# Performance work log

Measured on AMD Instinct MI355X. Metric: run time of the kernel, lower is better.

The kernel has to match this reference:

```python
import jax, jax.numpy as jnp
import numpy as np

N_NODES = 50000
N_EDGES = 800000
NUM_GRAPHS = 256
F_IN = 64        # num_features (per-head out dim == in dim in this module)
HEADS = 4        # n_heads1
OUT_DIM = 128    # output_dim
HC = HEADS * F_IN
NEG_SLOPE = 0.2  # GATConv leaky_relu slope
EPS = 1e-5       # GraphNorm eps


def setup_inputs() -> dict:
    key = jax.random.key(0)
    ks = jax.random.split(key, 12)
    s = lambda k, shape, fan: (jax.random.normal(k, shape, jnp.float32) / np.sqrt(fan).astype(np.float32))
    return {
        "x": jax.random.normal(ks[0], (N_NODES, F_IN), jnp.float32),
        "edge_index": jax.random.randint(ks[1], (2, N_EDGES), 0, N_NODES),
        "batch": jnp.sort(jax.random.randint(ks[2], (N_NODES,), 0, NUM_GRAPHS)),
        # GATConv params
        "lin_w": s(ks[3], (HC, F_IN), F_IN),
        "att_src": s(ks[4], (HEADS, F_IN), F_IN),
        "att_dst": s(ks[5], (HEADS, F_IN), F_IN),
        "gat_bias": jnp.zeros((HC,), jnp.float32),
        # GraphNorm params
        "gn_weight": jnp.ones((HC,), jnp.float32),
        "gn_bias": jnp.zeros((HC,), jnp.float32),
        "gn_mean_scale": jnp.ones((HC,), jnp.float32),
        # fc_g1 / out heads
        "fc1_w": s(ks[6], (OUT_DIM, HC), HC), "fc1_b": jnp.zeros((OUT_DIM,), jnp.float32),
        "out_w": s(ks[7], (1, OUT_DIM), OUT_DIM), "out_b": jnp.zeros((1,), jnp.float32),
        # GlobalAttention gate_nn: Linear(HC,16) -> ReLU -> Linear(16,1) -> Sigmoid
        "att1_w": s(ks[8], (16, HC), HC), "att1_b": jnp.zeros((16,), jnp.float32),
        "att2_w": s(ks[9], (1, 16), 16), "att2_b": jnp.zeros((1,), jnp.float32),
    }


def _gat_conv(x, edge_index, lin_w, att_src, att_dst, gat_bias):
    """PyG GATConv with add_self_loops=True, concat heads. Returns (out [N,HC], alpha [E+N,H])."""
    N = x.shape[0]
    xh = (x @ lin_w.T).reshape(N, HEADS, F_IN)                 # [N,H,C]
    a_src = (xh * att_src[None]).sum(-1)                        # [N,H]
    a_dst = (xh * att_dst[None]).sum(-1)                        # [N,H]
    loops = jnp.arange(N)
    src = jnp.concatenate([edge_index[0], loops])               # [E+N]
    dst = jnp.concatenate([edge_index[1], loops])
    alpha = jax.nn.leaky_relu(a_src[src] + a_dst[dst], NEG_SLOPE)  # [E+N,H]
    # segment softmax over incoming edges of each dst node (self-loops guarantee non-empty)
    amax = jax.ops.segment_max(alpha, dst, num_segments=N)
    alpha = jnp.exp(alpha - amax[dst])
    denom = jax.ops.segment_sum(alpha, dst, num_segments=N)
    alpha = alpha / (denom[dst] + 1e-16)
    msg = xh[src] * alpha[:, :, None]                           # [E+N,H,C]
    out = jax.ops.segment_sum(msg, dst, num_segments=N).reshape(N, HC) + gat_bias
    return out, alpha


def _graph_norm(x, batch, weight, bias, mean_scale):
    ones = jnp.ones((x.shape[0],), x.dtype)
    cnt = jnp.maximum(jax.ops.segment_sum(ones, batch, num_segments=NUM_GRAPHS), 1.0)[:, None]
    mean = jax.ops.segment_sum(x, batch, num_segments=NUM_GRAPHS) / cnt
    sub = x - mean[batch] * mean_scale
    var = jax.ops.segment_sum(sub * sub, batch, num_segments=NUM_GRAPHS) / cnt
    return weight * sub / jnp.sqrt(var + EPS)[batch] + bias


def _global_attention(x, batch, att1_w, att1_b, att2_w, att2_b):
    gate = jax.nn.sigmoid(jax.nn.relu(x @ att1_w.T + att1_b) @ att2_w.T + att2_b)  # [N,1]
    gmax = jax.ops.segment_max(gate, batch, num_segments=NUM_GRAPHS)
    gate = jnp.exp(gate - gmax[batch])
    gden = jax.ops.segment_sum(gate, batch, num_segments=NUM_GRAPHS)
    gate = gate / (gden[batch] + 1e-16)
    return jax.ops.segment_sum(gate * x, batch, num_segments=NUM_GRAPHS)  # [G,HC]


def reference(x, edge_index, batch, lin_w, att_src, att_dst, gat_bias,
              gn_weight, gn_bias, gn_mean_scale, fc1_w, fc1_b, out_w, out_b,
              att1_w, att1_b, att2_w, att2_b):
    x2, alpha = _gat_conv(x, edge_index, lin_w, att_src, att_dst, gat_bias)
    h = _graph_norm(x2, batch, gn_weight, gn_bias, gn_mean_scale)
    h = jax.nn.relu(h)                                # node_dropout = identity (eval)
    pooled = _global_attention(h, batch, att1_w, att1_b, att2_w, att2_b)
    h = jax.nn.relu(pooled @ fc1_w.T + fc1_b)          # dropout = identity (eval)
    out = jax.nn.sigmoid(h @ out_w.T + out_b)          # [G,1]
    return out, alpha
```

## Files before the change

### kernel.cpp

```cpp
#include <hip/hip_runtime.h>
#include <hip/hip_fp16.h>
#include <math.h>

#define NN 50000
#define NE 800000
#define NG 256
#define NEG_SLOPE 0.2f
#define GEPS 1e-5f
#define CHUNK 64
#define NB 196
#define CAP 6144
#define EPB 3125
#define SPLIT 8
#define NLINB 782
#define ABLK 3321

typedef _Float16 f16x8 __attribute__((ext_vector_type(8)));
typedef _Float16 f16x4 __attribute__((ext_vector_type(4)));
typedef float f32x4 __attribute__((ext_vector_type(4)));
typedef float f32x2 __attribute__((ext_vector_type(2)));

__device__ __forceinline__ float lrelu(float v){ return v > 0.f ? v : NEG_SLOPE * v; }

__global__ __launch_bounds__(256) void k_misc(const float* __restrict__ lin_w,
                                              _Float16* __restrict__ wh,
                                              const float* __restrict__ att1_w,
                                              _Float16* __restrict__ a1w,
                                              const int* __restrict__ batch,
                                              int* __restrict__ goff,
                                              int* __restrict__ gcnt,
                                              int* __restrict__ bucket_cnt) {
  int b = blockIdx.x, tid = threadIdx.x;
  if (b == 0) {
    if (tid < NB) bucket_cnt[tid] = 0;
    int g = tid;
    int lo = 0, hi = NN;
    while (lo < hi) { int mid = (lo + hi) >> 1; if (batch[mid] < g) lo = mid + 1; else hi = mid; }
    int start = lo;
    lo = 0; hi = NN;
    while (lo < hi) { int mid = (lo + hi) >> 1; if (batch[mid] < g + 1) lo = mid + 1; else hi = mid; }
    goff[g] = start;
    gcnt[g] = lo - start;
  } else if (b <= 16) {
    int i0 = (b - 1) * 1024 + tid * 4;
    float4 f = *(const float4*)&lin_w[i0];
    f16x4 h4;
    h4[0] = (_Float16)f.x; h4[1] = (_Float16)f.y; h4[2] = (_Float16)f.z; h4[3] = (_Float16)f.w;
    *(f16x4*)&wh[i0] = h4;
  } else {
    int i0 = (b - 17) * 1024 + tid * 4;
    float4 f = *(const float4*)&att1_w[i0];
    f16x4 h4;
    h4[0] = (_Float16)f.x; h4[1] = (_Float16)f.y; h4[2] = (_Float16)f.z; h4[3] = (_Float16)f.w;
    *(f16x4*)&a1w[i0] = h4;
  }
}

__device__ __forceinline__ void lin_body(char* smem,
                                         const float* __restrict__ x,
                                         const _Float16* __restrict__ wh,
                                         const float* __restrict__ att_src,
                                         const float* __restrict__ att_dst,
                                         unsigned char* __restrict__ xh8,
                                         float* __restrict__ a_src_n,
                                         float* __restrict__ a_dst_n) {
  unsigned char* s_f8 = (unsigned char*)smem;
  int w = threadIdx.x >> 6, lane = threadIdx.x & 63;
  int nb = blockIdx.x * 64 + w * 16;
  if (nb >= NN) return;
  int am = lane & 15, quad = lane >> 4;
  int wb = w * 4096;

  const float* xr = x + (size_t)(nb + am) * 64 + quad * 8;
  float4 f0 = *(const float4*)(xr);
  float4 f1 = *(const float4*)(xr + 4);
  float4 f2 = *(const float4*)(xr + 32);
  float4 f3 = *(const float4*)(xr + 36);
  f16x8 a0, a1;
  a0[0] = (_Float16)f0.x; a0[1] = (_Float16)f0.y; a0[2] = (_Float16)f0.z; a0[3] = (_Float16)f0.w;
  a0[4] = (_Float16)f1.x; a0[5] = (_Float16)f1.y; a0[6] = (_Float16)f1.z; a0[7] = (_Float16)f1.w;
  a1[0] = (_Float16)f2.x; a1[1] = (_Float16)f2.y; a1[2] = (_Float16)f2.z; a1[3] = (_Float16)f2.w;
  a1[4] = (_Float16)f3.x; a1[5] = (_Float16)f3.y; a1[6] = (_Float16)f3.z; a1[7] = (_Float16)f3.w;

  f32x4 acc[16];
#pragma unroll
  for (int ct = 0; ct < 16; ct++) acc[ct] = (f32x4){0.f, 0.f, 0.f, 0.f};

#pragma unroll
  for (int ct = 0; ct < 16; ct++) {
    const _Float16* wbp = wh + (size_t)(ct * 16 + am) * 64 + quad * 8;
    f16x8 b0 = *(const f16x8*)(wbp);
    f16x8 b1 = *(const f16x8*)(wbp + 32);
    acc[ct] = __builtin_amdgcn_mfma_f32_16x16x32_f16(a0, b0, acc[ct], 0, 0, 0);
    acc[ct] = __builtin_amdgcn_mfma_f32_16x16x32_f16(a1, b1, acc[ct], 0, 0, 0);
  }

  float ps[4][4], pd[4][4];
#pragma unroll
  for (int r = 0; r < 4; r++)
#pragma unroll
    for (int h = 0; h < 4; h++) { ps[r][h] = 0.f; pd[r][h] = 0.f; }
#pragma unroll
  for (int ct = 0; ct < 16; ct++) {
    int c = ct * 16 + am;
    float av = att_src[c];
    float dv = att_dst[c];
    int h = ct >> 2;
#pragma unroll
    for (int r = 0; r < 4; r++) {
      float v = acc[ct][r];
      ps[r][h] += v * av;
      pd[r][h] += v * dv;
    }
  }
#pragma unroll
  for (int r = 0; r < 4; r++)
#pragma unroll
    for (int h = 0; h < 4; h++) {
      float s = ps[r][h], d = pd[r][h];
#pragma unroll
      for (int o = 1; o < 16; o <<= 1) {
        s += __shfl_xor(s, o, 64);
        d += __shfl_xor(d, o, 64);
      }
      if (am == 0) {
        int node = nb + quad * 4 + r;
        a_src_n[node * 4 + h] = s;
        a_dst_n[node * 4 + h] = d;
      }
    }

#pragma unroll
  for (int r = 0; r < 4; r++) {
    uint4 u;
    int t;
    t = __builtin_amdgcn_cvt_pk_fp8_f32(acc[0][r],  acc[1][r],  0, 0);
    t = __builtin_amdgcn_cvt_pk_fp8_f32(acc[2][r],  acc[3][r],  t, 1);
    u.x = (unsigned)t;
    t = __builtin_amdgcn_cvt_pk_fp8_f32(acc[4][r],  acc[5][r],  0, 0);
    t = __builtin_amdgcn_cvt_pk_fp8_f32(acc[6][r],  acc[7][r],  t, 1);
    u.y = (unsigned)t;
    t = __builtin_amdgcn_cvt_pk_fp8_f32(acc[8][r],  acc[9][r],  0, 0);
    t = __builtin_amdgcn_cvt_pk_fp8_f32(acc[10][r], acc[11][r], t, 1);
    u.z = (unsigned)t;
    t = __builtin_amdgcn_cvt_pk_fp8_f32(acc[12][r], acc[13][r], 0, 0);
    t = __builtin_amdgcn_cvt_pk_fp8_f32(acc[14][r], acc[15][r], t, 1);
    u.w = (unsigned)t;
    *(uint4*)&s_f8[wb + (quad * 4 + r) * 256 + am * 16] = u;
  }
#pragma unroll
  for (int p = 0; p < 4; p++) {
    uint4 u = *(const uint4*)&s_f8[wb + p * 1024 + lane * 16];
    *(uint4*)&xh8[(size_t)nb * 256 + p * 1024 + lane * 16] = u;
  }
}

__device__ __forceinline__ void binA_body(char* smem, int b,
                                          const int* __restrict__ ei,
                                          int* __restrict__ bucket_cnt,
                                          int2* __restrict__ ebuf) {
  int2* sorted = (int2*)smem;
  int*  hist   = (int*)(smem + 25024);
  int*  lbase  = (int*)(smem + 25824);
  int*  cur    = (int*)(smem + 26624);
  int*  runb   = (int*)(smem + 27424);
  int*  wsum   = (int*)(smem + 28224);
  int tid = threadIdx.x, lane = tid & 63, wid = tid >> 6;
  int e0 = b * EPB, e1 = min(e0 + EPB, NE);
  int n = e1 - e0;
  for (int i = tid; i < NB; i += 256) hist[i] = 0;
  __syncthreads();
  for (int e = e0 + tid; e < e1; e += 256) atomicAdd(&hist[ei[NE + e] >> 8], 1);
  __syncthreads();
  {
    int v = (tid < NB) ? hist[tid] : 0;
    int s = v;
#pragma unroll
    for (int o = 1; o < 64; o <<= 1) { int t = __shfl_up(s, o, 64); if (lane >= o) s += t; }
    if (lane == 63) wsum[wid] = s;
    __syncthreads();
    int wbase = 0;
    for (int k = 0; k < wid; k++) wbase += wsum[k];
    if (tid < NB) {
      int ex = wbase + s - v;
      lbase[tid] = ex;
      cur[tid] = ex;
      runb[tid] = atomicAdd(&bucket_cnt[tid], v);
    }
  }
  __syncthreads();
  for (int e = e0 + tid; e < e1; e += 256) {
    int d = ei[NE + e], s = ei[e];
    int lp = atomicAdd(&cur[d >> 8], 1);
    sorted[lp] = make_int2(d, s);
  }
  __syncthreads();
  for (int i = tid; i < n; i += 256) {
    int2 e = sorted[i];
    int bk = e.x >> 8;
    int slot = runb[bk] + (i - lbase[bk]);
    if (slot < CAP) ebuf[(size_t)bk * CAP + slot] = e;
  }
}

__global__ __launch_bounds__(256) void k_linbin(const float* __restrict__ x,
                                                const _Float16* __restrict__ wh,
                                                const float* __restrict__ att_src,
                                                const float* __restrict__ att_dst,
                                                unsigned char* __restrict__ xh8,
                                                float* __restrict__ a_src_n,
                                                float* __restrict__ a_dst_n,
                                                const int* __restrict__ ei,
                                                int* __restrict__ bucket_cnt,
                                                int2* __restrict__ ebuf) {
  __shared__ __align__(16) char smem[28240];
  if (blockIdx.x < NLINB)
    lin_body(smem, x, wh, att_src, att_dst, xh8, a_src_n, a_dst_n);
  else
    binA_body(smem, blockIdx.x - NLINB, ei, bucket_cnt, ebuf);
}

__global__ __launch_bounds__(256) void k_binB(const int2* __restrict__ ebuf,
                                              const int* __restrict__ bucket_cnt,
                                              int* __restrict__ deg,
                                              int* __restrict__ offs,
                                              int* __restrict__ src_list) {
  __shared__ int hist[256];
  __shared__ int cur[256];
  __shared__ int wsum[4];
  __shared__ int bbase[NB];
  int b = blockIdx.x, tid = threadIdx.x, lane = tid & 63, wid = tid >> 6;
  {
    int v = (tid < NB) ? min(bucket_cnt[tid], CAP) : 0;
    int s = v;
#pragma unroll
    for (int o = 1; o < 64; o <<= 1) { int t = __shfl_up(s, o, 64); if (lane >= o) s += t; }
    if (lane == 63) wsum[wid] = s;
    __syncthreads();
    int wbase = 0;
    for (int k = 0; k < wid; k++) wbase += wsum[k];
    if (tid < NB) bbase[tid] = wbase + s - v;
  }
  __syncthreads();
  int cnt = min(bucket_cnt[b], CAP);
  int base = bbase[b];
  const int2* seg = ebuf + (size_t)b * CAP;
  hist[tid] = 0;
  __syncthreads();
  for (int i = tid; i < cnt; i += 256) atomicAdd(&hist[seg[i].x & 255], 1);
  __syncthreads();
  int v = hist[tid];
  int s = v;
#pragma unroll
  for (int o = 1; o < 64; o <<= 1) { int t = __shfl_up(s, o, 64); if (lane >= o) s += t; }
  if (lane == 63) wsum[wid] = s;
  __syncthreads();
  int wbase = 0;
  for (int k = 0; k < wid; k++) wbase += wsum[k];
  int excl = wbase + s - v;
  int node = b * 256 + tid;
  if (node < NN) {
    deg[node] = v;
    offs[node] = base + excl;
  }
  cur[tid] = excl;
  __syncthreads();
  for (int i = tid; i < cnt; i += 256) {
    int2 e = seg[i];
    int pos = base + atomicAdd(&cur[e.x & 255], 1);
    src_list[pos] = e.y;
  }
}

__global__ __launch_bounds__(64) void k_gat(const unsigned char* __restrict__ xh8,
                                            const float* __restrict__ a_src_n,
                                            const float* __restrict__ a_dst_n,
                                            const int* __restrict__ offs,
                                            const int* __restrict__ deg_arr,
                                            const int* __restrict__ src_list,
                                            const float* __restrict__ gat_bias,
                                            __half* __restrict__ x2h,
                                            float* __restrict__ den_inv) {
  __shared__ __align__(16) float s_al[CHUNK * 4];
  __shared__ int s_src[CHUNK];
  __shared__ __half s_tr[256];
  int n = blockIdx.x, lane = threadIdx.x;
  int off = offs[n], dg = deg_arr[n], cnt = dg + 1;
  float4 ad = *(const float4*)&a_dst_n[n * 4];
  int h = lane & 3;
  unsigned loff = 4u * (unsigned)lane;
  float acc0 = 0.f, acc1 = 0.f, acc2 = 0.f, acc3 = 0.f;

  if (cnt <= 64) {
    float e0 = 0.f, e1 = 0.f, e2 = 0.f, e3 = 0.f;
    if (lane < cnt) {
      int src = (lane < dg) ? src_list[off + lane] : n;
      float4 as = *(const float4*)&a_src_n[src * 4];
      e0 = __expf(lrelu(as.x + ad.x));
      e1 = __expf(lrelu(as.y + ad.y));
      e2 = __expf(lrelu(as.z + ad.z));
      e3 = __expf(lrelu(as.w + ad.w));
      s_src[lane] = src;
    }
    float s0 = e0, s1 = e1, s2 = e2, s3 = e3;
#pragma unroll
    for (int o = 32; o >= 1; o >>= 1) {
      s0 += __shfl_xor(s0, o, 64);
      s1 += __shfl_xor(s1, o, 64);
      s2 += __shfl_xor(s2, o, 64);
      s3 += __shfl_xor(s3, o, 64);
    }
    float i0 = 1.f / (s0 + 1e-16f), i1 = 1.f / (s1 + 1e-16f);
    float i2 = 1.f / (s2 + 1e-16f), i3 = 1.f / (s3 + 1e-16f);
    if (lane == 0) *(float4*)&den_inv[n * 4] = make_float4(i0, i1, i2, i3);
    if (lane < cnt) {
      s_al[lane * 4 + 0] = e0 * i0;
      s_al[lane * 4 + 1] = e1 * i1;
      s_al[lane * 4 + 2] = e2 * i2;
      s_al[lane * 4 + 3] = e3 * i3;
    }
    __syncthreads();
    int j = 0;
    for (; j + 4 <= cnt; j += 4) {
      unsigned oA = ((unsigned)s_src[j] << 8) + loff;
      unsigned oB = ((unsigned)s_src[j + 1] << 8) + loff;
      unsigned oC = ((unsigned)s_src[j + 2] << 8) + loff;
      unsigned oD = ((unsigned)s_src[j + 3] << 8) + loff;
      unsigned rA = *(const unsigned*)&xh8[oA];
      unsigned rB = *(const unsigned*)&xh8[oB];
      unsigned rC = *(const unsigned*)&xh8[oC];
      unsigned rD = *(const unsigned*)&xh8[oD];
      float aA = s_al[j * 4 + h], aB = s_al[(j + 1) * 4 + h];
      float aC = s_al[(j + 2) * 4 + h], aD = s_al[(j + 3) * 4 + h];
      f32x2 lA = __builtin_amdgcn_cvt_pk_f32_fp8((int)rA, 0);
      f32x2 hA = __builtin_amdgcn_cvt_pk_f32_fp8((int)rA, 1);
      f32x2 lB = __builtin_amdgcn_cvt_pk_f32_fp8((int)rB, 0);
      f32x2 hB = __builtin_amdgcn_cvt_pk_f32_fp8((int)rB, 1);
      f32x2 lC = __builtin_amdgcn_cvt_pk_f32_fp8((int)rC, 0);
      f32x2 hC = __builtin_amdgcn_cvt_pk_f32_fp8((int)rC, 1);
      f32x2 lD = __builtin_amdgcn_cvt_pk_f32_fp8((int)rD, 0);
      f32x2 hD = __builtin_amdgcn_cvt_pk_f32_fp8((int)rD, 1);
      acc0 += aA * lA[0] + aB * lB[0] + aC * lC[0] + aD * lD[0];
      acc1 += aA * lA[1] + aB * lB[1] + aC * lC[1] + aD * lD[1];
      acc2 += aA * hA[0] + aB * hB[0] + aC * hC[0] + aD * hD[0];
      acc3 += aA * hA[1] + aB * hB[1] + aC * hC[1] + aD * hD[1];
    }
    for (; j < cnt; j++) {
      unsigned oA = ((unsigned)s_src[j] << 8) + loff;
      unsigned rA = *(const unsigned*)&xh8[oA];
      float aA = s_al[j * 4 + h];
      f32x2 lA = __builtin_amdgcn_cvt_pk_f32_fp8((int)rA, 0);
      f32x2 hA = __builtin_amdgcn_cvt_pk_f32_fp8((int)rA, 1);
      acc0 += aA * lA[0];
      acc1 += aA * lA[1];
      acc2 += aA * hA[0];
      acc3 += aA * hA[1];
    }
  } else {
    float s0 = 0.f, s1 = 0.f, s2 = 0.f, s3 = 0.f;
    for (int j = lane; j < cnt; j += 64) {
      int src = (j < dg) ? src_list[off + j] : n;
      float4 as = *(const float4*)&a_src_n[src * 4];
      s0 += __expf(lrelu(as.x + ad.x));
      s1 += __expf(lrelu(as.y + ad.y));
      s2 += __expf(lrelu(as.z + ad.z));
      s3 += __expf(lrelu(as.w + ad.w));
    }
#pragma unroll
    for (int o = 32; o >= 1; o >>= 1) {
      s0 += __shfl_xor(s0, o, 64);
      s1 += __shfl_xor(s1, o, 64);
      s2 += __shfl_xor(s2, o, 64);
      s3 += __shfl_xor(s3, o, 64);
    }
    float i0 = 1.f / (s0 + 1e-16f), i1 = 1.f / (s1 + 1e-16f);
    float i2 = 1.f / (s2 + 1e-16f), i3 = 1.f / (s3 + 1e-16f);
    if (lane == 0) *(float4*)&den_inv[n * 4] = make_float4(i0, i1, i2, i3);
    for (int cb = 0; cb < cnt; cb += CHUNK) {
      int clen = min(CHUNK, cnt - cb);
      for (int j = lane; j < clen; j += 64) {
        int jj = cb + j;
        int src = (jj < dg) ? src_list[off + jj] : n;
        float4 as = *(const float4*)&a_src_n[src * 4];
        s_src[j] = src;
        s_al[j * 4 + 0] = __expf(lrelu(as.x + ad.x)) * i0;
        s_al[j * 4 + 1] = __expf(lrelu(as.y + ad.y)) * i1;
        s_al[j * 4 + 2] = __expf(lrelu(as.z + ad.z)) * i2;
        s_al[j * 4 + 3] = __expf(lrelu(as.w + ad.w)) * i3;
      }
      __syncthreads();
      for (int j = 0; j < clen; j++) {
        unsigned oA = ((unsigned)s_src[j] << 8) + loff;
        unsigned rA = *(const unsigned*)&xh8[oA];
        float aA = s_al[j * 4 + h];
        f32x2 lA = __builtin_amdgcn_cvt_pk_f32_fp8((int)rA, 0);
        f32x2 hA = __builtin_amdgcn_cvt_pk_f32_fp8((int)rA, 1);
        acc0 += aA * lA[0];
        acc1 += aA * lA[1];
        acc2 += aA * hA[0];
        acc3 += aA * hA[1];
      }
      __syncthreads();
    }
  }

  int cb0 = (lane & 3) * 64 + (lane >> 2);
  s_tr[cb0 +  0] = __float2half(acc0 + gat_bias[cb0 +  0]);
  s_tr[cb0 + 16] = __float2half(acc1 + gat_bias[cb0 + 16]);
  s_tr[cb0 + 32] = __float2half(acc2 + gat_bias[cb0 + 32]);
  s_tr[cb0 + 48] = __float2half(acc3 + gat_bias[cb0 + 48]);
  __syncthreads();
  uint2 u = *(const uint2*)&s_tr[4 * lane];
  *(uint2*)&x2h[(size_t)n * 256 + 4 * lane] = u;
}

__global__ __launch_bounds__(256) void k_alst(const int* __restrict__ ei,
                                              const float* __restrict__ a_src_n,
                                              const float* __restrict__ a_dst_n,
                                              const float* __restrict__ den_inv,
                                              float* __restrict__ alpha_out,
                                              const __half* __restrict__ x2h,
                                              const int* __restrict__ gcnt,
                                              const int* __restrict__ goff,
                                              float* __restrict__ psumA,
                                              float* __restrict__ psumB) {
  if (blockIdx.x < ABLK) {
    int idx = blockIdx.x * 256 + threadIdx.x;
    if (idx >= NE + NN) return;
    int s, d;
    if (idx < NE) { s = ei[idx]; d = ei[NE + idx]; }
    else          { s = idx - NE; d = s; }
    float4 as = *(const float4*)&a_src_n[s * 4];
    float4 ad = *(const float4*)&a_dst_n[d * 4];
    float4 iv = *(const float4*)&den_inv[d * 4];
    float4 a;
    a.x = __expf(lrelu(as.x + ad.x)) * iv.x;
    a.y = __expf(lrelu(as.y + ad.y)) * iv.y;
    a.z = __expf(lrelu(as.z + ad.z)) * iv.z;
    a.w = __expf(lrelu(as.w + ad.w)) * iv.w;
    *(float4*)&alpha_out[(size_t)idx * 4] = a;
  } else {
    int b = blockIdx.x - ABLK, c = threadIdx.x;
    int g = b >> 3, s = b & 7;
    int cnt = gcnt[g], start = goff[g];
    const __half* p = x2h + (size_t)start * 256 + c;
    float sum = 0.f, sum2 = 0.f;
    int i = s;
    for (; i + 56 < cnt; i += 64) {
      float v0 = __half2float(p[(size_t)(i +  0) * 256]);
      float v1 = __half2float(p[(size_t)(i +  8) * 256]);
      float v2 = __half2float(p[(size_t)(i + 16) * 256]);
      float v3 = __half2float(p[(size_t)(i + 24) * 256]);
      float v4 = __half2float(p[(size_t)(i + 32) * 256]);
      float v5 = __half2float(p[(size_t)(i + 40) * 256]);
      float v6 = __half2float(p[(size_t)(i + 48) * 256]);
      float v7 = __half2float(p[(size_t)(i + 56) * 256]);
      sum += ((v0 + v1) + (v2 + v3)) + ((v4 + v5) + (v6 + v7));
      sum2 += ((v0 * v0 + v1 * v1) + (v2 * v2 + v3 * v3)) +
              ((v4 * v4 + v5 * v5) + (v6 * v6 + v7 * v7));
    }
    for (; i < cnt; i += 8) { float v = __half2float(p[(size_t)i * 256]); sum += v; sum2 += v * v; }
    psumA[b * 256 + c] = sum;
    psumB[b * 256 + c] = sum2;
  }
}

__global__ __launch_bounds__(256) void k_stats2(const float* __restrict__ psumA,
                                                const float* __restrict__ psumB,
                                                const int* __restrict__ gcnt,
                                                const float* __restrict__ gn_w,
                                                const float* __restrict__ gn_b,
                                                const float* __restrict__ gn_ms,
                                                float* __restrict__ scale_g,
                                                float* __restrict__ shift_g) {
  int g = blockIdx.x, c = threadIdx.x;
  int b0 = g * SPLIT;
  float S = 0.f, S2 = 0.f;
#pragma unroll
  for (int k = 0; k < SPLIT; k++) {
    S  += psumA[(b0 + k) * 256 + c];
    S2 += psumB[(b0 + k) * 256 + c];
  }
  float fc = fmaxf((float)gcnt[g], 1.f);
  float mean = S / fc;
  float mm = mean * gn_ms[c];
  float var = fmaxf(S2 / fc - 2.f * mm * mean + mm * mm, 0.f);
  float sc = gn_w[c] / sqrtf(var + GEPS);
  scale_g[g * 256 + c] = sc;
  shift_g[g * 256 + c] = gn_b[c] - sc * mm;
}

__global__ __launch_bounds__(256) void k_gate(const __half* __restrict__ x2h,
                                              const int* __restrict__ batch,
                                              const float* __restrict__ scale_g,
                                              const float* __restrict__ shift_g,
                                              const _Float16* __restrict__ a1w,
                                              const float* __restrict__ att1_b,
                                              const float* __restrict__ att2_w,
                                              const float* __restrict__ att2_b,
                                              float* __restrict__ gate_raw) {
  int w = threadIdx.x >> 6, lane = threadIdx.x & 63;
  int nb = blockIdx.x * 64 + w * 16;
  if (nb >= NN) return;
  int am = lane & 15, quad = lane >> 4;
  int node = nb + am;
  int g = batch[node];

  const __half*   xp  = x2h + (size_t)node * 256 + quad * 8;
  const float*    scp = scale_g + g * 256 + quad * 8;
  const float*    shp = shift_g + g * 256 + quad * 8;
  const _Float16* bp  = a1w + am * 256 + quad * 8;

  f32x4 acc = (f32x4){0.f, 0.f, 0.f, 0.f};
#pragma unroll
  for (int kb = 0; kb < 8; kb++) {
    f16x8 xv = *(const f16x8*)(xp + kb * 32);
    float4 sc0 = *(const float4*)(scp + kb * 32);
    float4 sc1 = *(const float4*)(scp + kb * 32 + 4);
    float4 sh0 = *(const float4*)(shp + kb * 32);
    float4 sh1 = *(const float4*)(shp + kb * 32 + 4);
    f16x8 a;
    a[0] = (_Float16)fmaxf(sc0.x * (float)xv[0] + sh0.x, 0.f);
    a[1] = (_Float16)fmaxf(sc0.y * (float)xv[1] + sh0.y, 0.f);
    a[2] = (_Float16)fmaxf(sc0.z * (float)xv[2] + sh0.z, 0.f);
    a[3] = (_Float16)fmaxf(sc0.w * (float)xv[3] + sh0.w, 0.f);
    a[4] = (_Float16)fmaxf(sc1.x * (float)xv[4] + sh1.x, 0.f);
    a[5] = (_Float16)fmaxf(sc1.y * (float)xv[5] + sh1.y, 0.f);
    a[6] = (_Float16)fmaxf(sc1.z * (float)xv[6] + sh1.z, 0.f);
    a[7] = (_Float16)fmaxf(sc1.w * (float)xv[7] + sh1.w, 0.f);
    f16x8 b = *(const f16x8*)(bp + kb * 32);
    acc = __builtin_amdgcn_mfma_f32_16x16x32_f16(a, b, acc, 0, 0, 0);
  }

  float b1 = att1_b[am], w2 = att2_w[am], b2 = att2_b[0];
#pragma unroll
  for (int r = 0; r < 4; r++) {
    float t = w2 * fmaxf(acc[r] + b1, 0.f);
#pragma unroll
    for (int o = 1; o < 16; o <<= 1) t += __shfl_xor(t, o, 64);
    if (am == 0) gate_raw[nb + quad * 4 + r] = 1.f / (1.f + __expf(-(t + b2)));
  }
}

__global__ __launch_bounds__(256) void k_poolp(const __half* __restrict__ x2h,
                                               const float* __restrict__ gate_raw,
                                               const int* __restrict__ gcnt,
                                               const int* __restrict__ goff,
                                               const float* __restrict__ scale_g,
                                               const float* __restrict__ shift_g,
                                               float* __restrict__ ppool) {
  __shared__ float s_w[1024];
  __shared__ float red[4];
  int b = blockIdx.x, c = threadIdx.x, lane = c & 63, wid = c >> 6;
  int g = b >> 3, s = b & 7;
  int cnt = gcnt[g], start = goff[g];
  float ls = 0.f;
  for (int i = c; i < cnt; i += 256) {
    float e = __expf(gate_raw[start + i]);
    s_w[i] = e;
    ls += e;
  }
#pragma unroll
  for (int o = 32; o >= 1; o >>= 1) ls += __shfl_xor(ls, o, 64);
  if (lane == 0) red[wid] = ls;
  __syncthreads();
  float rden = 1.f / (red[0] + red[1] + red[2] + red[3] + 1e-16f);

  float sc = scale_g[g * 256 + c], sh = shift_g[g * 256 + c];
  const __half* p = x2h + (size_t)start * 256 + c;
  float pooled = 0.f;
  int i = s;
  for (; i + 56 < cnt; i += 64) {
    float v0 = __half2float(p[(size_t)(i +  0) * 256]);
    float v1 = __half2float(p[(size_t)(i +  8) * 256]);
    float v2 = __half2float(p[(size_t)(i + 16) * 256]);
    float v3 = __half2float(p[(size_t)(i + 24) * 256]);
    float v4 = __half2float(p[(size_t)(i + 32) * 256]);
    float v5 = __half2float(p[(size_t)(i + 40) * 256]);
    float v6 = __half2float(p[(size_t)(i + 48) * 256]);
    float v7 = __half2float(p[(size_t)(i + 56) * 256]);
    pooled += s_w[i +  0] * fmaxf(sc * v0 + sh, 0.f);
    pooled += s_w[i +  8] * fmaxf(sc * v1 + sh, 0.f);
    pooled += s_w[i + 16] * fmaxf(sc * v2 + sh, 0.f);
    pooled += s_w[i + 24] * fmaxf(sc * v3 + sh, 0.f);
    pooled += s_w[i + 32] * fmaxf(sc * v4 + sh, 0.f);
    pooled += s_w[i + 40] * fmaxf(sc * v5 + sh, 0.f);
    pooled += s_w[i + 48] * fmaxf(sc * v6 + sh, 0.f);
    pooled += s_w[i + 56] * fmaxf(sc * v7 + sh, 0.f);
  }
  for (; i < cnt; i += 8)
    pooled += s_w[i] * fmaxf(sc * __half2float(p[(size_t)i * 256]) + sh, 0.f);
  ppool[b * 256 + c] = pooled * rden;
}

__global__ __launch_bounds__(256) void k_fin(const float* __restrict__ ppool,
                                             const float* __restrict__ fc1_w,
                                             const float* __restrict__ fc1_b,
                                             const float* __restrict__ out_w,
                                             const float* __restrict__ out_b,
                                             float* __restrict__ outp) {
  __shared__ __align__(16) float pool_s[256];
  __shared__ float hred[128];
  __shared__ float red[4];
  int g = blockIdx.x, tid = threadIdx.x, lane = tid & 63, wid = tid >> 6;
  int b0 = g * SPLIT;
  float acc = 0.f;
#pragma unroll
  for (int k = 0; k < SPLIT; k++) acc += ppool[(b0 + k) * 256 + tid];
  pool_s[tid] = acc;
  __syncthreads();
  float4 psv = *(const float4*)&pool_s[4 * lane];
  for (int j0 = 0; j0 < 32; j0++) {
    int j = wid * 32 + j0;
    float4 w = *(const float4*)&fc1_w[j * 256 + 4 * lane];
    float d = w.x * psv.x + w.y * psv.y + w.z * psv.z + w.w * psv.w;
#pragma unroll
    for (int o = 32; o >= 1; o >>= 1) d += __shfl_xor(d, o, 64);
    if (lane == 0) hred[j] = fmaxf(d + fc1_b[j], 0.f) * out_w[j];
  }
  __syncthreads();
  if (tid < 128) {
    float v = hred[tid];
#pragma unroll
    for (int o = 32; o >= 1; o >>= 1) v += __shfl_xor(v, o, 64);
    if (lane == 0) red[wid] = v;
  }
  __syncthreads();
  if (tid == 0) outp[g] = 1.f / (1.f + __expf(-(red[0] + red[1] + out_b[0])));
}

extern "C" void kernel_launch(void* const* d_in, const int* in_sizes, int n_in,
                              void* d_out, int out_size, void* d_ws, size_t ws_size,
                              hipStream_t stream) {
  const float* x        = (const float*)d_in[0];
  const int*   ei       = (const int*)d_in[1];
  const int*   batch    = (const int*)d_in[2];
  const float* lin_w    = (const float*)d_in[3];
  const float* att_src  = (const float*)d_in[4];
  const float* att_dst  = (const float*)d_in[5];
  const float* gat_bias = (const float*)d_in[6];
  const float* gn_w     = (const float*)d_in[7];
  const float* gn_b     = (const float*)d_in[8];
  const float* gn_ms    = (const float*)d_in[9];
  const float* fc1_w    = (const float*)d_in[10];
  const float* fc1_b    = (const float*)d_in[11];
  const float* out_w    = (const float*)d_in[12];
  const float* out_b    = (const float*)d_in[13];
  const float* att1_w   = (const float*)d_in[14];
  const float* att1_b   = (const float*)d_in[15];
  const float* att2_w   = (const float*)d_in[16];
  const float* att2_b   = (const float*)d_in[17];

  float* outp  = (float*)d_out;
  float* alpha = outp + NG;

  char* wsb = (char*)d_ws;
  size_t o = 0;
  auto A = [&](size_t bytes) -> char* {
    char* p = wsb + o;
    o += (bytes + 255) & ~(size_t)255;
    return p;
  };
  unsigned char* xh8 = (unsigned char*)A((size_t)NN * 256);
  __half*   x2h      = (__half*)A((size_t)NN * 256 * 2);
  _Float16* wh       = (_Float16*)A((size_t)256 * 64 * 2);
  _Float16* a1w      = (_Float16*)A((size_t)16 * 256 * 2);
  float* a_src_n  = (float*)A((size_t)NN * 4 * 4);
  float* a_dst_n  = (float*)A((size_t)NN * 4 * 4);
  float* den_inv  = (float*)A((size_t)NN * 4 * 4);
  float* gate_raw = (float*)A((size_t)NN * 4);
  float* psumA    = (float*)A((size_t)NG * SPLIT * 256 * 4);
  float* psumB    = (float*)A((size_t)NG * SPLIT * 256 * 4);
  float* ppool    = (float*)A((size_t)NG * SPLIT * 256 * 4);
  float* scale_g  = (float*)A((size_t)NG * 256 * 4);
  float* shift_g  = (float*)A((size_t)NG * 256 * 4);
  int*   deg      = (int*)A((size_t)NN * 4);
  int*   gcnt     = (int*)A((size_t)NG * 4);
  int*   offs     = (int*)A((size_t)NN * 4);
  int*   goff     = (int*)A((size_t)NG * 4);
  int*   src_list = (int*)A((size_t)NE * 4);
  int2*  ebuf     = (int2*)A((size_t)NB * CAP * 8);
  int*   bucket_cnt  = (int*)A((size_t)NB * 4);

  k_misc<<<21, 256, 0, stream>>>(lin_w, wh, att1_w, a1w, batch, goff, gcnt, bucket_cnt);
  k_linbin<<<NLINB + 256, 256, 0, stream>>>(x, wh, att_src, att_dst, xh8, a_src_n, a_dst_n,
                                            ei, bucket_cnt, ebuf);
  k_binB<<<NB, 256, 0, stream>>>(ebuf, bucket_cnt, deg, offs, src_list);
  k_gat<<<NN, 64, 0, stream>>>(xh8, a_src_n, a_dst_n, offs, deg, src_list,
                               gat_bias, x2h, den_inv);
  k_alst<<<ABLK + NG * SPLIT, 256, 0, stream>>>(ei, a_src_n, a_dst_n, den_inv, alpha,
                                                x2h, gcnt, goff, psumA, psumB);
  k_stats2<<<NG, 256, 0, stream>>>(psumA, psumB, gcnt, gn_w, gn_b, gn_ms, scale_g, shift_g);
  k_gate<<<(NN + 63) / 64, 256, 0, stream>>>(x2h, batch, scale_g, shift_g, a1w, att1_b,
                                             att2_w, att2_b, gate_raw);
  k_poolp<<<NG * SPLIT, 256, 0, stream>>>(x2h, gate_raw, gcnt, goff, scale_g, shift_g, ppool);
  k_fin<<<NG, 256, 0, stream>>>(ppool, fc1_w, fc1_b, out_w, out_b, outp);
}
```

Before: 248.4 us.

## Restructure GAT aggregation: 16-byte gathers, 4 edges per step, deferred softmax normalization

Rewrites the per-node GAT aggregation kernel so each lane gathers 16 bytes of fp8 features per edge, with 16 lanes covering a row and 4 edge groups processed in parallel. Partial sums are reduced across groups with shuffles at the end. Softmax normalization is deferred: unnormalized exponentials are accumulated and scaled by the inverse denominator at the end, which merges the small-degree and large-degree paths into one single-pass loop. The intent is fewer, wider gather loads and removal of the second pass over sources for high-degree nodes, at the cost of more accumulator registers and an extra cross-lane reduction.

```diff
diff --git a/kernel.cpp b/kernel.cpp
--- a/kernel.cpp
+++ b/kernel.cpp
@@ -7,7 +7,6 @@
 #define NG 256
 #define NEG_SLOPE 0.2f
 #define GEPS 1e-5f
-#define CHUNK 64
 #define NB 196
 #define CAP 6144
 #define EPB 3125
@@ -281,134 +280,91 @@
                                             const float* __restrict__ gat_bias,
                                             __half* __restrict__ x2h,
                                             float* __restrict__ den_inv) {
-  __shared__ __align__(16) float s_al[CHUNK * 4];
-  __shared__ int s_src[CHUNK];
+  __shared__ __align__(16) float s_al[64 * 4];
+  __shared__ int s_src[64];
   __shared__ __half s_tr[256];
   int n = blockIdx.x, lane = threadIdx.x;
   int off = offs[n], dg = deg_arr[n], cnt = dg + 1;
   float4 ad = *(const float4*)&a_dst_n[n * 4];
-  int h = lane & 3;
-  unsigned loff = 4u * (unsigned)lane;
-  float acc0 = 0.f, acc1 = 0.f, acc2 = 0.f, acc3 = 0.f;
-
-  if (cnt <= 64) {
-    float e0 = 0.f, e1 = 0.f, e2 = 0.f, e3 = 0.f;
-    if (lane < cnt) {
-      int src = (lane < dg) ? src_list[off + lane] : n;
+  int am = lane & 15, eg = lane >> 4;
+  unsigned loff = (unsigned)am * 16u;
+
+  f32x4 acc[4];
+#pragma unroll
+  for (int w = 0; w < 4; w++) acc[w] = (f32x4){0.f, 0.f, 0.f, 0.f};
+  float s0 = 0.f, s1 = 0.f, s2 = 0.f, s3 = 0.f;
+
+  for (int cb = 0; cb < cnt; cb += 64) {
+    int clen = min(64, cnt - cb);
+    int pad = (clen + 3) & ~3;
+    if (lane < clen) {
+      int j = cb + lane;
+      int src = (j < dg) ? src_list[off + j] : n;
       float4 as = *(const float4*)&a_src_n[src * 4];
-      e0 = __expf(lrelu(as.x + ad.x));
-      e1 = __expf(lrelu(as.y + ad.y));
-      e2 = __expf(lrelu(as.z + ad.z));
-      e3 = __expf(lrelu(as.w + ad.w));
+      float e0 = __expf(lrelu(as.x + ad.x));
+      float e1 = __expf(lrelu(as.y + ad.y));
+      float e2 = __expf(lrelu(as.z + ad.z));
+      float e3 = __expf(lrelu(as.w + ad.w));
       s_src[lane] = src;
-    }
-    float s0 = e0, s1 = e1, s2 = e2, s3 = e3;
-#pragma unroll
-    for (int o = 32; o >= 1; o >>= 1) {
-      s0 += __shfl_xor(s0, o, 64);
-      s1 += __shfl_xor(s1, o, 64);
-      s2 += __shfl_xor(s2, o, 64);
-      s3 += __shfl_xor(s3, o, 64);
-    }
-    float i0 = 1.f / (s0 + 1e-16f), i1 = 1.f / (s1 + 1e-16f);
-    float i2 = 1.f / (s2 + 1e-16f), i3 = 1.f / (s3 + 1e-16f);
-    if (lane == 0) *(float4*)&den_inv[n * 4] = make_float4(i0, i1, i2, i3);
-    if (lane < cnt) {
-      s_al[lane * 4 + 0] = e0 * i0;
-      s_al[lane * 4 + 1] = e1 * i1;
-      s_al[lane * 4 + 2] = e2 * i2;
-      s_al[lane * 4 + 3] = e3 * i3;
+      *(float4*)&s_al[lane * 4] = make_float4(e0, e1, e2, e3);
+      s0 += e0; s1 += e1; s2 += e2; s3 += e3;
+    } else if (lane < pad) {
+      s_src[lane] = n;
+      *(float4*)&s_al[lane * 4] = make_float4(0.f, 0.f, 0.f, 0.f);
     }
     __syncthreads();
-    int j = 0;
-    for (; j + 4 <= cnt; j += 4) {
-      unsigned oA = ((unsigned)s_src[j] << 8) + loff;
-      unsigned oB = ((unsigned)s_src[j + 1] << 8) + loff;
-      unsigned oC = ((unsigned)s_src[j + 2] << 8) + loff;
-      unsigned oD = ((unsigned)s_src[j + 3] << 8) + loff;
-      unsigned rA = *(const unsigned*)&xh8[oA];
-      unsigned rB = *(const unsigned*)&xh8[oB];
-      unsigned rC = *(const unsigned*)&xh8[oC];
-      unsigned rD = *(const unsigned*)&xh8[oD];
-      float aA = s_al[j * 4 + h], aB = s_al[(j + 1) * 4 + h];
-      float aC = s_al[(j + 2) * 4 + h], aD = s_al[(j + 3) * 4 + h];
-      f32x2 lA = __builtin_amdgcn_cvt_pk_f32_fp8((int)rA, 0);
-      f32x2 hA = __builtin_amdgcn_cvt_pk_f32_fp8((int)rA, 1);
-      f32x2 lB = __builtin_amdgcn_cvt_pk_f32_fp8((int)rB, 0);
-      f32x2 hB = __builtin_amdgcn_cvt_pk_f32_fp8((int)rB, 1);
-      f32x2 lC = __builtin_amdgcn_cvt_pk_f32_fp8((int)rC, 0);
-      f32x2 hC = __builtin_amdgcn_cvt_pk_f32_fp8((int)rC, 1);
-      f32x2 lD = __builtin_amdgcn_cvt_pk_f32_fp8((int)rD, 0);
-      f32x2 hD = __builtin_amdgcn_cvt_pk_f32_fp8((int)rD, 1);
-      acc0 += aA * lA[0] + aB * lB[0] + aC * lC[0] + aD * lD[0];
-      acc1 += aA * lA[1] + aB * lB[1] + aC * lC[1] + aD * lD[1];
-      acc2 += aA * hA[0] + aB * hB[0] + aC * hC[0] + aD * hD[0];
-      acc3 += aA * hA[1] + aB * hB[1] + aC * hC[1] + aD * hD[1];
+    for (int j = 0; j < pad; j += 4) {
+      int e = j + eg;
+      unsigned oA = ((unsigned)s_src[e] << 8) + loff;
+      uint4 r = *(const uint4*)&xh8[oA];
+      float4 a4 = *(const float4*)&s_al[e * 4];
+      f32x2 l0 = __builtin_amdgcn_cvt_pk_f32_fp8((int)r.x, 0);
+      f32x2 h0 = __builtin_amdgcn_cvt_pk_f32_fp8((int)r.x, 1);
+      f32x2 l1 = __builtin_amdgcn_cvt_pk_f32_fp8((int)r.y, 0);
+      f32x2 h1 = __builtin_amdgcn_cvt_pk_f32_fp8((int)r.y, 1);
+      f32x2 l2 = __builtin_amdgcn_cvt_pk_f32_fp8((int)r.z, 0);
+      f32x2 h2 = __builtin_amdgcn_cvt_pk_f32_fp8((int)r.z, 1);
+      f32x2 l3 = __builtin_amdgcn_cvt_pk_f32_fp8((int)r.w, 0);
+      f32x2 h3 = __builtin_amdgcn_cvt_pk_f32_fp8((int)r.w, 1);
+      acc[0][0] += a4.x * l0[0]; acc[0][1] += a4.x * l0[1];
+      acc[0][2] += a4.x * h0[0]; acc[0][3] += a4.x * h0[1];
+      acc[1][0] += a4.y * l1[0]; acc[1][1] += a4.y * l1[1];
+      acc[1][2] += a4.y * h1[0]; acc[1][3] += a4.y * h1[1];
+      acc[2][0] += a4.z * l2[0]; acc[2][1] += a4.z * l2[1];
+      acc[2][2] += a4.z * h2[0]; acc[2][3] += a4.z * h2[1];
+      acc[3][0] += a4.w * l3[0]; acc[3][1] += a4.w * l3[1];
+      acc[3][2] += a4.w * h3[0]; acc[3][3] += a4.w * h3[1];
     }
-    for (; j < cnt; j++) {
-      unsigned oA = ((unsigned)s_src[j] << 8) + loff;
-      unsigned rA = *(const unsigned*)&xh8[oA];
-      float aA = s_al[j * 4 + h];
-      f32x2 lA = __builtin_amdgcn_cvt_pk_f32_fp8((int)rA, 0);
-      f32x2 hA = __builtin_amdgcn_cvt_pk_f32_fp8((int)rA, 1);
-      acc0 += aA * lA[0];
-      acc1 += aA * lA[1];
-      acc2 += aA * hA[0];
-      acc3 += aA * hA[1];
+    __syncthreads();
+  }
+
+#pragma unroll
+  for (int o = 32; o >= 1; o >>= 1) {
+    s0 += __shfl_xor(s0, o, 64);
+    s1 += __shfl_xor(s1, o, 64);
+    s2 += __shfl_xor(s2, o, 64);
+    s3 += __shfl_xor(s3, o, 64);
+  }
+  float i0 = 1.f / (s0 + 1e-16f), i1 = 1.f / (s1 + 1e-16f);
+  float i2 = 1.f / (s2 + 1e-16f), i3 = 1.f / (s3 + 1e-16f);
+  if (lane == 0) *(float4*)&den_inv[n * 4] = make_float4(i0, i1, i2, i3);
+
+#pragma unroll
+  for (int w = 0; w < 4; w++)
+#pragma unroll
+    for (int k = 0; k < 4; k++) {
+      float v = acc[w][k];
+      v += __shfl_xor(v, 16, 64);
+      v += __shfl_xor(v, 32, 64);
+      acc[w][k] = v;
     }
-  } else {
-    float s0 = 0.f, s1 = 0.f, s2 = 0.f, s3 = 0.f;
-    for (int j = lane; j < cnt; j += 64) {
-      int src = (j < dg) ? src_list[off + j] : n;
-      float4 as = *(const float4*)&a_src_n[src * 4];
-      s0 += __expf(lrelu(as.x + ad.x));
-      s1 += __expf(lrelu(as.y + ad.y));
-      s2 += __expf(lrelu(as.z + ad.z));
-      s3 += __expf(lrelu(as.w + ad.w));
-    }
-#pragma unroll
-    for (int o = 32; o >= 1; o >>= 1) {
-      s0 += __shfl_xor(s0, o, 64);
-      s1 += __shfl_xor(s1, o, 64);
-      s2 += __shfl_xor(s2, o, 64);
-      s3 += __shfl_xor(s3, o, 64);
-    }
-    float i0 = 1.f / (s0 + 1e-16f), i1 = 1.f / (s1 + 1e-16f);
-    float i2 = 1.f / (s2 + 1e-16f), i3 = 1.f / (s3 + 1e-16f);
-    if (lane == 0) *(float4*)&den_inv[n * 4] = make_float4(i0, i1, i2, i3);
-    for (int cb = 0; cb < cnt; cb += CHUNK) {
-      int clen = min(CHUNK, cnt - cb);
-      for (int j = lane; j < clen; j += 64) {
-        int jj = cb + j;
-        int src = (jj < dg) ? src_list[off + jj] : n;
-        float4 as = *(const float4*)&a_src_n[src * 4];
-        s_src[j] = src;
-        s_al[j * 4 + 0] = __expf(lrelu(as.x + ad.x)) * i0;
-        s_al[j * 4 + 1] = __expf(lrelu(as.y + ad.y)) * i1;
-        s_al[j * 4 + 2] = __expf(lrelu(as.z + ad.z)) * i2;
-        s_al[j * 4 + 3] = __expf(lrelu(as.w + ad.w)) * i3;
-      }
-      __syncthreads();
-      for (int j = 0; j < clen; j++) {
-        unsigned oA = ((unsigned)s_src[j] << 8) + loff;
-        unsigned rA = *(const unsigned*)&xh8[oA];
-        float aA = s_al[j * 4 + h];
-        f32x2 lA = __builtin_amdgcn_cvt_pk_f32_fp8((int)rA, 0);
-        f32x2 hA = __builtin_amdgcn_cvt_pk_f32_fp8((int)rA, 1);
-        acc0 += aA * lA[0];
-        acc1 += aA * lA[1];
-        acc2 += aA * hA[0];
-        acc3 += aA * hA[1];
-      }
-      __syncthreads();
-    }
-  }
-
-  int cb0 = (lane & 3) * 64 + (lane >> 2);
-  s_tr[cb0 +  0] = __float2half(acc0 + gat_bias[cb0 +  0]);
-  s_tr[cb0 + 16] = __float2half(acc1 + gat_bias[cb0 + 16]);
-  s_tr[cb0 + 32] = __float2half(acc2 + gat_bias[cb0 + 32]);
-  s_tr[cb0 + 48] = __float2half(acc3 + gat_bias[cb0 + 48]);
+
+  float ivw = (eg == 0) ? i0 : (eg == 1) ? i1 : (eg == 2) ? i2 : i3;
+#pragma unroll
+  for (int k = 0; k < 4; k++) {
+    int c = (4 * eg + k) * 16 + am;
+    s_tr[c] = __float2half(acc[eg][k] * ivw + gat_bias[c]);
+  }
   __syncthreads();
   uint2 u = *(const uint2*)&s_tr[4 * lane];
   *(uint2*)&x2h[(size_t)n * 256 + 4 * lane] = u;
```

Result: slower. 266.4 us (+7.3%).
